# Optimization experiments

Measured on AMD Instinct MI355X. Metric: run time of the kernel, lower is better.

The kernel has to match this reference:

```python
import jax, jax.numpy as jnp
import numpy as np

D_MODEL = 1024
D_STATE = 16
LN_EPS = 1e-5


def setup_inputs() -> dict:
    key = jax.random.key(0)
    ks = jax.random.split(key, 8)
    batch, seq_len = 8, 4096
    x = jax.random.normal(ks[0], (batch, seq_len, D_MODEL), dtype=jnp.float32)
    A = jax.random.normal(ks[1], (D_STATE, D_STATE), dtype=jnp.float32) * 0.01
    # nn.Linear default init: U(-1/sqrt(fan_in), 1/sqrt(fan_in))
    bb = 1.0 / np.sqrt(D_MODEL)
    B_w = jax.random.uniform(ks[2], (D_STATE, D_MODEL), minval=-bb, maxval=bb)
    B_b = jax.random.uniform(ks[3], (D_STATE,), minval=-bb, maxval=bb)
    cb = 1.0 / np.sqrt(D_STATE)
    C_w = jax.random.uniform(ks[4], (D_MODEL, D_STATE), minval=-cb, maxval=cb)
    C_b = jax.random.uniform(ks[5], (D_MODEL,), minval=-cb, maxval=cb)
    D = jnp.ones((D_MODEL,), dtype=jnp.float32) * 0.01
    gate_w = jax.random.uniform(ks[6], (D_MODEL, D_MODEL), minval=-bb, maxval=bb)
    gate_b = jax.random.uniform(ks[7], (D_MODEL,), minval=-bb, maxval=bb)
    ln_g = jnp.ones((D_MODEL,), dtype=jnp.float32)
    ln_b = jnp.zeros((D_MODEL,), dtype=jnp.float32)
    return {"x": x, "A": A, "B_w": B_w, "B_b": B_b, "C_w": C_w, "C_b": C_b,
            "D": D, "gate_w": gate_w, "gate_b": gate_b, "ln_g": ln_g, "ln_b": ln_b}


def _layer_norm(z, g, b):
    mu = jnp.mean(z, axis=-1, keepdims=True)
    var = jnp.mean(jnp.square(z - mu), axis=-1, keepdims=True)
    return (z - mu) * jax.lax.rsqrt(var + LN_EPS) * g + b


def reference(x, A, B_w, B_b, C_w, C_b, D, gate_w, gate_b, ln_g, ln_b):
    batch, seq_len, d_model = x.shape
    # Precompute B(x_t) for all t in one GEMM: [b, s, d_state]
    Bx = jnp.einsum('bsd,nd->bsn', x, B_w) + B_b

    def step(state, bx_t):  # state: [b, d_state], bx_t: [b, d_state]
        new_state = jnp.tanh(state @ A.T + bx_t)
        return new_state, new_state

    init = jnp.zeros((batch, A.shape[0]), dtype=x.dtype)
    _, states = jax.lax.scan(step, init, jnp.swapaxes(Bx, 0, 1))  # [s, b, n]
    states = jnp.swapaxes(states, 0, 1)  # [b, s, d_state]

    output = jnp.einsum('bsn,dn->bsd', states, C_w) + C_b + D * x
    gate = jax.nn.silu(jnp.einsum('bsd,ed->bse', x, gate_w) + gate_b)
    output = gate * output + (1.0 - gate) * x
    return _layer_norm(output + x, ln_g, ln_b)
```

## Files before the change

kernel.cpp:

```cpp
#include <hip/hip_runtime.h>
#include <hip/hip_bf16.h>
#include <cstdint>
#include <cstddef>

#define DM     1024
#define DSTATE 16
#define SEQ    4096
#define BATCH  8
#define MROWS  (BATCH * SEQ)
#define LNEPS  1e-5f

#define CHUNK  64
#define WARM   16
#define NCHUNK (SEQ / CHUNK)

typedef __hip_bfloat16 bf16;
typedef __attribute__((ext_vector_type(8))) short short8;
typedef __attribute__((ext_vector_type(4))) float f32x4;

static __device__ __forceinline__ unsigned short f2bf(float f) {
  bf16 h = __float2bfloat16(f);
  return __builtin_bit_cast(unsigned short, h);
}

#define GLDS16(SRC, DSTOFF, LDSBASE)                                          \
  __builtin_amdgcn_global_load_lds(                                           \
      (const __attribute__((address_space(1))) void*)(SRC),                   \
      (__attribute__((address_space(3))) void*)((LDSBASE) + (DSTOFF)), 16, 0, 0)

#define WAITV(N) asm volatile("s_waitcnt vmcnt(" #N ")" ::: "memory")

#define XBLK (MROWS * DM / (256 * 8))
#define GBLK (DM * DM / (256 * 8))

__global__ __launch_bounds__(256) void canon_all(const float* __restrict__ xin,
                                                 const float* __restrict__ gw,
                                                 bf16* __restrict__ wsx,
                                                 bf16* __restrict__ gwc) {
  int blk = blockIdx.x;
  const float* src;
  bf16* dst;
  size_t i;
  if (blk < XBLK) {
    i = ((size_t)blk * 256 + threadIdx.x) * 8;
    src = xin; dst = wsx;
  } else {
    i = ((size_t)(blk - XBLK) * 256 + threadIdx.x) * 8;
    src = gw; dst = gwc;
  }
  const float4* p = (const float4*)(src + i);
  float4 a = p[0], b = p[1];
  uint4 o;
  o.x = (unsigned)f2bf(a.x) | ((unsigned)f2bf(a.y) << 16);
  o.y = (unsigned)f2bf(a.z) | ((unsigned)f2bf(a.w) << 16);
  o.z = (unsigned)f2bf(b.x) | ((unsigned)f2bf(b.y) << 16);
  o.w = (unsigned)f2bf(b.z) | ((unsigned)f2bf(b.w) << 16);
  *(uint4*)(dst + i) = o;
}

__global__ __launch_bounds__(256) void bx_kernel(const bf16* __restrict__ X,
                                                 const float* __restrict__ Bw,
                                                 const float* __restrict__ Bb,
                                                 float* __restrict__ Bx) {
  __shared__ __align__(16) char lds[40960];
  const int tid  = threadIdx.x;
  const int lane = tid & 63;
  const int w    = tid >> 6;
  const int fm   = lane & 15;
  const int fq   = lane >> 4;
  const int l4   = lane >> 2, lk = lane & 3;
  const int m0   = blockIdx.x * 64;

  {
    int t6   = tid & 63;
    int nb   = tid >> 6;
    int step = t6 >> 1;
    int cq0  = (t6 & 1) * 2;
#pragma unroll
    for (int p = 0; p < 4; ++p) {
      int n = p * 4 + nb;
      const float4* src = (const float4*)(Bw + (size_t)n * DM + t6 * 16);
      float4 a = src[0], b = src[1], c = src[2], d = src[3];
      uint4 o0, o1;
      o0.x = (unsigned)f2bf(a.x) | ((unsigned)f2bf(a.y) << 16);
      o0.y = (unsigned)f2bf(a.z) | ((unsigned)f2bf(a.w) << 16);
      o0.z = (unsigned)f2bf(b.x) | ((unsigned)f2bf(b.y) << 16);
      o0.w = (unsigned)f2bf(b.z) | ((unsigned)f2bf(b.w) << 16);
      o1.x = (unsigned)f2bf(c.x) | ((unsigned)f2bf(c.y) << 16);
      o1.y = (unsigned)f2bf(c.z) | ((unsigned)f2bf(c.w) << 16);
      o1.z = (unsigned)f2bf(d.x) | ((unsigned)f2bf(d.y) << 16);
      o1.w = (unsigned)f2bf(d.z) | ((unsigned)f2bf(d.w) << 16);
      int sw = (n >> 1) & 3;
      *(uint4*)(lds + step * 1024 + n * 64 + ((cq0 ^ sw) << 4))       = o0;
      *(uint4*)(lds + step * 1024 + n * 64 + (((cq0 + 1) ^ sw) << 4)) = o1;
    }
  }

  const int rowA = w * 16 + l4;
  const int kqA  = lk ^ ((rowA >> 1) & 3);
  GLDS16(X + (size_t)(m0 + rowA) * DM + kqA * 8, 32768 + w * 1024, lds);
  __syncthreads();

  const int rA   = w * 16 + fm;
  const int offA = rA * 64 + ((fq ^ ((rA >> 1) & 3)) << 4);
  const int offB = fm * 64 + ((fq ^ ((fm >> 1) & 3)) << 4);

  f32x4 acc = (f32x4)(0.f);
  for (int t = 0; t < 32; ++t) {
    const int cb = 32768 + (t & 1) * 4096;
    const int sb = 32768 + 4096 - (t & 1) * 4096;
    if (t < 31) {
      GLDS16(X + (size_t)(m0 + rowA) * DM + (t + 1) * 32 + kqA * 8,
             sb + w * 1024, lds);
      WAITV(1);
    } else {
      WAITV(0);
    }
    __builtin_amdgcn_s_barrier();
    __builtin_amdgcn_sched_barrier(0);
    short8 af  = *(const short8*)(lds + cb + offA);
    short8 bfv = *(const short8*)(lds + t * 1024 + offB);
    acc = __builtin_amdgcn_mfma_f32_16x16x32_bf16(af, bfv, acc, 0, 0, 0);
    __builtin_amdgcn_s_barrier();
  }
  float bb = Bb[fm];
#pragma unroll
  for (int q = 0; q < 4; ++q) {
    int row = m0 + w * 16 + fq * 4 + q;
    Bx[(size_t)row * DSTATE + fm] = acc[q] + bb;
  }
}

__global__ __launch_bounds__(64) void scan_kernel(const float* __restrict__ A,
                                                  const float* __restrict__ Bx,
                                                  float* __restrict__ st) {
  int lane = threadIdx.x;
  int n    = lane & 15;
  int base = lane & 48;
  int chain = blockIdx.x * 4 + (lane >> 4);
  int c = chain >> 3;
  int b = chain & 7;

  float Arow[16];
#pragma unroll
  for (int m = 0; m < 16; m++) Arow[m] = A[n * 16 + m];

  int t0   = (c == 0) ? 0 : c * CHUNK - WARM;
  int t1   = c * CHUNK;
  int tEnd = c * CHUNK + CHUNK;

  const float* bxp = Bx + (size_t)b * SEQ * DSTATE + n;
  float*       stp = st + (size_t)b * SEQ * DSTATE + n;

  float state = 0.f;
  for (int t = t0; t < tEnd; t++) {
    float a = bxp[(size_t)t * DSTATE];
#pragma unroll
    for (int m = 0; m < 16; m++)
      a += Arow[m] * __shfl(state, base + m, 64);
    float e = __expf(-2.f * fabsf(a));
    float r = (1.f - e) / (1.f + e);
    state = __builtin_copysignf(r, a);
    if (t >= t1) stp[(size_t)t * DSTATE] = state;
  }
}

#define FBM 32
#define FBK 32
#define NT  (DM / FBK)
#define BUFB 67584
#define CW_OFF 0
#define ST_OFF 65536
#define PART_OFF 67584
#define TOT_OFF 69632
#define BOUNCE 71680

__global__ __launch_bounds__(512, 2) void fused_kernel(
    const bf16* __restrict__ X, const bf16* __restrict__ Gw,
    const float* __restrict__ xf, const float* __restrict__ st,
    const float* __restrict__ Cw, const float* __restrict__ Cb,
    const float* __restrict__ Dv, const float* __restrict__ gb,
    const float* __restrict__ lng, const float* __restrict__ lnb,
    float* __restrict__ out) {
  __shared__ __align__(16) char lds[137216];
  const int tid  = threadIdx.x;
  const int lane = tid & 63;
  const int w    = tid >> 6;
  const int fm   = lane & 15;
  const int fq   = lane >> 4;
  const int m0   = blockIdx.x * FBM;
  const int l4   = lane >> 2, lk = lane & 3;

  int colS[8], kqS[8];
#pragma unroll
  for (int s = 0; s < 8; s++) {
    int col = (w * 8 + s) * 16 + l4;
    colS[s] = col;
    kqS[s]  = lk ^ ((col >> 1) & 3);
  }
  const int rowA = w * 16 + l4;
  const int kqA  = lk ^ ((rowA >> 1) & 3);

  int offA[2], offB[8];
#pragma unroll
  for (int i = 0; i < 2; i++) {
    int r = i * 16 + fm;
    offA[i] = r * 64 + ((fq ^ ((r >> 1) & 3)) << 4);
  }
#pragma unroll
  for (int j = 0; j < 8; j++) {
    int c = w * 128 + j * 16 + fm;
    offB[j] = 2048 + c * 64 + ((fq ^ ((c >> 1) & 3)) << 4);
  }

  f32x4 acc[2][8];
#pragma unroll
  for (int i = 0; i < 2; i++)
#pragma unroll
    for (int j = 0; j < 8; j++) acc[i][j] = (f32x4)(0.f);

  {
#pragma unroll
    for (int s = 0; s < 8; s++)
      GLDS16(Gw + (size_t)colS[s] * DM + kqS[s] * 8,
             2048 + (w * 8 + s) * 1024, lds);
    if (w < 2)
      GLDS16(X + (size_t)(m0 + rowA) * DM + kqA * 8, w * 1024, lds);
  }

  for (int t = 0; t < NT; t++) {
    const int cb = (t & 1) * BUFB;
    const int sb = BUFB - cb;
    if (t < NT - 1) {
      const int kb = (t + 1) * FBK;
#pragma unroll
      for (int s = 0; s < 8; s++)
        GLDS16(Gw + (size_t)colS[s] * DM + kb + kqS[s] * 8,
               sb + 2048 + (w * 8 + s) * 1024, lds);
      if (w < 2)
        GLDS16(X + (size_t)(m0 + rowA) * DM + kb + kqA * 8, sb + w * 1024, lds);
    } else {
#pragma unroll
      for (int s = 0; s < 8; s++) {
        int c   = w * 8 + s;
        int col = c * 16 + l4;
        int nq  = lk ^ ((col >> 1) & 3);
        GLDS16(Cw + (size_t)col * DSTATE + nq * 4, CW_OFF + c * 1024, lds);
      }
      if (w < 2) {
        int cc  = w;
        int row = cc * 16 + l4;
        int nq  = lk ^ ((row >> 1) & 3);
        GLDS16(st + (size_t)(m0 + row) * DSTATE + nq * 4, ST_OFF + cc * 1024, lds);
      }
    }

    if (w < 2) WAITV(9); else WAITV(8);
    __builtin_amdgcn_s_barrier();
    __builtin_amdgcn_sched_barrier(0);

    short8 af[2];
#pragma unroll
    for (int i = 0; i < 2; i++) af[i] = *(const short8*)(lds + cb + offA[i]);
#pragma unroll
    for (int j = 0; j < 8; j++) {
      short8 bfj = *(const short8*)(lds + cb + offB[j]);
#pragma unroll
      for (int i = 0; i < 2; i++)
        acc[i][j] = __builtin_amdgcn_mfma_f32_16x16x32_bf16(af[i], bfj,
                                                            acc[i][j], 0, 0, 0);
    }
    __builtin_amdgcn_s_barrier();
  }
  __syncthreads();

#pragma unroll
  for (int i = 0; i < 2; i++) {
    f32x4 stv[4][4];
#pragma unroll
    for (int nq = 0; nq < 4; nq++)
#pragma unroll
      for (int r = 0; r < 4; r++) {
        int row = i * 16 + fq * 4 + r;
        stv[nq][r] = *(const f32x4*)(lds + ST_OFF + row * 64 +
                                     ((nq ^ ((row >> 1) & 3)) << 4));
      }
    float sum4[4] = {0.f, 0.f, 0.f, 0.f};
    float ssq4[4] = {0.f, 0.f, 0.f, 0.f};
#pragma unroll
    for (int j = 0; j < 8; j++) {
      int c = w * 128 + j * 16 + fm;
      float oc[4] = {0.f, 0.f, 0.f, 0.f};
#pragma unroll
      for (int nq = 0; nq < 4; nq++) {
        f32x4 cw = *(const f32x4*)(lds + CW_OFF + c * 64 +
                                   ((nq ^ ((c >> 1) & 3)) << 4));
#pragma unroll
        for (int r = 0; r < 4; r++)
          oc[r] += stv[nq][r][0] * cw[0] + stv[nq][r][1] * cw[1] +
                   stv[nq][r][2] * cw[2] + stv[nq][r][3] * cw[3];
      }
      float gbv = gb[c], cbv = Cb[c], dvv = Dv[c];
#pragma unroll
      for (int r = 0; r < 4; r++) {
        int   grow = m0 + i * 16 + fq * 4 + r;
        float xv = xf[(size_t)grow * DM + c];
        float zg = acc[i][j][r] + gbv;
        float g  = zg / (1.f + __expf(-zg));
        float ocf = oc[r] + cbv + dvv * xv;
        float y  = g * ocf + (1.f - g) * xv;
        float z2 = y + xv;
        acc[i][j][r] = z2;
        sum4[r] += z2;
        ssq4[r] += z2 * z2;
      }
    }
#pragma unroll
    for (int r = 0; r < 4; r++) {
#pragma unroll
      for (int off = 1; off < 16; off <<= 1) {
        sum4[r] += __shfl_xor(sum4[r], off, 64);
        ssq4[r] += __shfl_xor(ssq4[r], off, 64);
      }
    }
    if (fm == 0) {
#pragma unroll
      for (int r = 0; r < 4; r++) {
        int row = i * 16 + fq * 4 + r;
        *(float2*)(lds + PART_OFF + w * 256 + row * 8) =
            make_float2(sum4[r], ssq4[r]);
      }
    }
  }
  __syncthreads();

  if (tid < 32) {
    float s = 0.f, q = 0.f;
#pragma unroll
    for (int ww = 0; ww < 8; ww++) {
      float2 p = *(const float2*)(lds + PART_OFF + ww * 256 + tid * 8);
      s += p.x; q += p.y;
    }
    float mu  = s * (1.f / DM);
    float var = q * (1.f / DM) - mu * mu;
    *(float2*)(lds + TOT_OFF + tid * 8) = make_float2(mu, rsqrtf(var + LNEPS));
  }
  __syncthreads();

  for (int h = 0; h < 2; ++h) {
#pragma unroll
    for (int j = 0; j < 8; ++j) {
      int c = w * 128 + j * 16 + fm;
#pragma unroll
      for (int r = 0; r < 4; ++r) {
        int row16 = fq * 4 + r;
        *(float*)(lds + BOUNCE + row16 * 4096 + c * 4) = acc[h][j][r];
      }
    }
    __syncthreads();
    {
      int row16 = tid >> 5;
      int lbase = (tid & 31) * 4;
      float2 mi = *(const float2*)(lds + TOT_OFF + (h * 16 + row16) * 8);
#pragma unroll
      for (int q = 0; q < 8; ++q) {
        int col = lbase + q * 128;
        f32x4 z = *(const f32x4*)(lds + BOUNCE + row16 * 4096 + col * 4);
        float4 g4 = *(const float4*)(lng + col);
        float4 b4 = *(const float4*)(lnb + col);
        float4 ov;
        ov.x = (z[0] - mi.x) * mi.y * g4.x + b4.x;
        ov.y = (z[1] - mi.x) * mi.y * g4.y + b4.y;
        ov.z = (z[2] - mi.x) * mi.y * g4.z + b4.z;
        ov.w = (z[3] - mi.x) * mi.y * g4.w + b4.w;
        *(float4*)(out + (size_t)(m0 + h * 16 + row16) * DM + col) = ov;
      }
    }
    __syncthreads();
  }
}

extern "C" void kernel_launch(void* const* d_in, const int* in_sizes, int n_in,
                              void* d_out, int out_size, void* d_ws, size_t ws_size,
                              hipStream_t stream) {
  (void)in_sizes; (void)n_in;
  const float* x   = (const float*)d_in[0];
  const float* A   = (const float*)d_in[1];
  const float* Bw  = (const float*)d_in[2];
  const float* Bb  = (const float*)d_in[3];
  const float* Cw  = (const float*)d_in[4];
  const float* Cb  = (const float*)d_in[5];
  const float* Dv  = (const float*)d_in[6];
  const float* Gw  = (const float*)d_in[7];
  const float* gb  = (const float*)d_in[8];
  const float* lng = (const float*)d_in[9];
  const float* lnb = (const float*)d_in[10];
  float* out = (float*)d_out;

  const size_t NEED = (size_t)72 << 20;
  if (ws_size < NEED) {
    hipMemsetAsync(d_out, 0, (size_t)out_size * 4, stream);
    return;
  }

  char* ws = (char*)d_ws;
  bf16*  wsx = (bf16*)(ws);
  bf16*  gwc = (bf16*)(ws + ((size_t)64 << 20));
  float* Bx  = (float*)(ws + ((size_t)66 << 20));
  float* st  = (float*)(ws + ((size_t)68 << 20));

  canon_all<<<XBLK + GBLK, 256, 0, stream>>>(x, Gw, wsx, gwc);
  bx_kernel<<<MROWS / 64, 256, 0, stream>>>(wsx, Bw, Bb, Bx);
  scan_kernel<<<(BATCH * NCHUNK) / 4, 64, 0, stream>>>(A, Bx, st);
  fused_kernel<<<MROWS / FBM, 512, 0, stream>>>(
      wsx, gwc, x, st, Cw, Cb, Dv, gb, lng, lnb, out);
}
```

Measured before the change: 500.0 us.

## Double fused GEMM row tile with 1024-thread blocks, halve scan chunk

The fused gate GEMM/epilogue kernel now processes 64 rows per block with 16 waves arranged as 2 row groups by 8 column groups. Each gate-weight K-slice loaded into LDS is shared by twice as many rows, which halves total weight traffic. In exchange, occupancy drops to one 1024-thread block per CU and the LN epilogue gets more passes. The scan chunk shrinks to 32, doubling parallel chains at the cost of more warm-up overhead. The bx kernel's explicit vmcnt wait plus double barrier is replaced by a single __syncthreads, which looks like it may drop the wait for the async global-to-LDS load.

```diff
diff --git a/kernel.cpp b/kernel.cpp
--- a/kernel.cpp
+++ b/kernel.cpp
@@ -10,7 +10,7 @@
 #define MROWS  (BATCH * SEQ)
 #define LNEPS  1e-5f
 
-#define CHUNK  64
+#define CHUNK  32
 #define WARM   16
 #define NCHUNK (SEQ / CHUNK)
 
@@ -109,19 +109,13 @@
   for (int t = 0; t < 32; ++t) {
     const int cb = 32768 + (t & 1) * 4096;
     const int sb = 32768 + 4096 - (t & 1) * 4096;
-    if (t < 31) {
+    if (t < 31)
       GLDS16(X + (size_t)(m0 + rowA) * DM + (t + 1) * 32 + kqA * 8,
              sb + w * 1024, lds);
-      WAITV(1);
-    } else {
-      WAITV(0);
-    }
-    __builtin_amdgcn_s_barrier();
-    __builtin_amdgcn_sched_barrier(0);
     short8 af  = *(const short8*)(lds + cb + offA);
     short8 bfv = *(const short8*)(lds + t * 1024 + offB);
     acc = __builtin_amdgcn_mfma_f32_16x16x32_bf16(af, bfv, acc, 0, 0, 0);
-    __builtin_amdgcn_s_barrier();
+    __syncthreads();
   }
   float bb = Bb[fm];
 #pragma unroll
@@ -165,36 +159,38 @@
   }
 }
 
-#define FBM 32
+#define FBM 64
 #define FBK 32
 #define NT  (DM / FBK)
-#define BUFB 67584
+#define BUFB 69632
 #define CW_OFF 0
 #define ST_OFF 65536
-#define PART_OFF 67584
-#define TOT_OFF 69632
-#define BOUNCE 71680
-
-__global__ __launch_bounds__(512, 2) void fused_kernel(
+#define BOUNCE 69632
+#define PART_OFF 139264
+#define TOT_OFF 143360
+
+__global__ __launch_bounds__(1024, 1) void fused_kernel(
     const bf16* __restrict__ X, const bf16* __restrict__ Gw,
     const float* __restrict__ xf, const float* __restrict__ st,
     const float* __restrict__ Cw, const float* __restrict__ Cb,
     const float* __restrict__ Dv, const float* __restrict__ gb,
     const float* __restrict__ lng, const float* __restrict__ lnb,
     float* __restrict__ out) {
-  __shared__ __align__(16) char lds[137216];
+  __shared__ __align__(16) char lds[143872];
   const int tid  = threadIdx.x;
   const int lane = tid & 63;
   const int w    = tid >> 6;
+  const int wr   = w >> 3;
+  const int wc   = w & 7;
   const int fm   = lane & 15;
   const int fq   = lane >> 4;
   const int m0   = blockIdx.x * FBM;
   const int l4   = lane >> 2, lk = lane & 3;
 
-  int colS[8], kqS[8];
-#pragma unroll
-  for (int s = 0; s < 8; s++) {
-    int col = (w * 8 + s) * 16 + l4;
+  int colS[4], kqS[4];
+#pragma unroll
+  for (int s = 0; s < 4; s++) {
+    int col = (w * 4 + s) * 16 + l4;
     colS[s] = col;
     kqS[s]  = lk ^ ((col >> 1) & 3);
   }
@@ -204,13 +200,13 @@
   int offA[2], offB[8];
 #pragma unroll
   for (int i = 0; i < 2; i++) {
-    int r = i * 16 + fm;
+    int r = wr * 32 + i * 16 + fm;
     offA[i] = r * 64 + ((fq ^ ((r >> 1) & 3)) << 4);
   }
 #pragma unroll
   for (int j = 0; j < 8; j++) {
-    int c = w * 128 + j * 16 + fm;
-    offB[j] = 2048 + c * 64 + ((fq ^ ((c >> 1) & 3)) << 4);
+    int c = wc * 128 + j * 16 + fm;
+    offB[j] = 4096 + c * 64 + ((fq ^ ((c >> 1) & 3)) << 4);
   }
 
   f32x4 acc[2][8];
@@ -221,10 +217,10 @@
 
   {
 #pragma unroll
-    for (int s = 0; s < 8; s++)
+    for (int s = 0; s < 4; s++)
       GLDS16(Gw + (size_t)colS[s] * DM + kqS[s] * 8,
-             2048 + (w * 8 + s) * 1024, lds);
-    if (w < 2)
+             4096 + (w * 4 + s) * 1024, lds);
+    if (w < 4)
       GLDS16(X + (size_t)(m0 + rowA) * DM + kqA * 8, w * 1024, lds);
   }
 
@@ -234,28 +230,27 @@
     if (t < NT - 1) {
       const int kb = (t + 1) * FBK;
 #pragma unroll
-      for (int s = 0; s < 8; s++)
+      for (int s = 0; s < 4; s++)
         GLDS16(Gw + (size_t)colS[s] * DM + kb + kqS[s] * 8,
-               sb + 2048 + (w * 8 + s) * 1024, lds);
-      if (w < 2)
+               sb + 4096 + (w * 4 + s) * 1024, lds);
+      if (w < 4)
         GLDS16(X + (size_t)(m0 + rowA) * DM + kb + kqA * 8, sb + w * 1024, lds);
     } else {
 #pragma unroll
-      for (int s = 0; s < 8; s++) {
-        int c   = w * 8 + s;
+      for (int s = 0; s < 4; s++) {
+        int c   = w * 4 + s;
         int col = c * 16 + l4;
         int nq  = lk ^ ((col >> 1) & 3);
         GLDS16(Cw + (size_t)col * DSTATE + nq * 4, CW_OFF + c * 1024, lds);
       }
-      if (w < 2) {
-        int cc  = w;
-        int row = cc * 16 + l4;
+      if (w < 4) {
+        int row = w * 16 + l4;
         int nq  = lk ^ ((row >> 1) & 3);
-        GLDS16(st + (size_t)(m0 + row) * DSTATE + nq * 4, ST_OFF + cc * 1024, lds);
-      }
-    }
-
-    if (w < 2) WAITV(9); else WAITV(8);
+        GLDS16(st + (size_t)(m0 + row) * DSTATE + nq * 4, ST_OFF + w * 1024, lds);
+      }
+    }
+
+    if (w < 4) WAITV(5); else WAITV(4);
     __builtin_amdgcn_s_barrier();
     __builtin_amdgcn_sched_barrier(0);
 
@@ -281,7 +276,7 @@
     for (int nq = 0; nq < 4; nq++)
 #pragma unroll
       for (int r = 0; r < 4; r++) {
-        int row = i * 16 + fq * 4 + r;
+        int row = wr * 32 + i * 16 + fq * 4 + r;
         stv[nq][r] = *(const f32x4*)(lds + ST_OFF + row * 64 +
                                      ((nq ^ ((row >> 1) & 3)) << 4));
       }
@@ -289,7 +284,7 @@
     float ssq4[4] = {0.f, 0.f, 0.f, 0.f};
 #pragma unroll
     for (int j = 0; j < 8; j++) {
-      int c = w * 128 + j * 16 + fm;
+      int c = wc * 128 + j * 16 + fm;
       float oc[4] = {0.f, 0.f, 0.f, 0.f};
 #pragma unroll
       for (int nq = 0; nq < 4; nq++) {
@@ -303,7 +298,7 @@
       float gbv = gb[c], cbv = Cb[c], dvv = Dv[c];
 #pragma unroll
       for (int r = 0; r < 4; r++) {
-        int   grow = m0 + i * 16 + fq * 4 + r;
+        int   grow = m0 + wr * 32 + i * 16 + fq * 4 + r;
         float xv = xf[(size_t)grow * DM + c];
         float zg = acc[i][j][r] + gbv;
         float g  = zg / (1.f + __expf(-zg));
@@ -334,11 +329,13 @@
   }
   __syncthreads();
 
-  if (tid < 32) {
+  if (tid < 64) {
+    int rw = tid >> 5;
     float s = 0.f, q = 0.f;
 #pragma unroll
-    for (int ww = 0; ww < 8; ww++) {
-      float2 p = *(const float2*)(lds + PART_OFF + ww * 256 + tid * 8);
+    for (int cc = 0; cc < 8; cc++) {
+      float2 p = *(const float2*)(lds + PART_OFF + (rw * 8 + cc) * 256 +
+                                  (tid & 31) * 8);
       s += p.x; q += p.y;
     }
     float mu  = s * (1.f / DM);
@@ -347,24 +344,27 @@
   }
   __syncthreads();
 
-  for (int h = 0; h < 2; ++h) {
-#pragma unroll
-    for (int j = 0; j < 8; ++j) {
-      int c = w * 128 + j * 16 + fm;
-#pragma unroll
-      for (int r = 0; r < 4; ++r) {
-        int row16 = fq * 4 + r;
-        *(float*)(lds + BOUNCE + row16 * 4096 + c * 4) = acc[h][j][r];
+  for (int h = 0; h < 4; ++h) {
+    if (wr == (h >> 1)) {
+      int i = h & 1;
+#pragma unroll
+      for (int j = 0; j < 8; ++j) {
+        int c = wc * 128 + j * 16 + fm;
+#pragma unroll
+        for (int r = 0; r < 4; ++r) {
+          int row16 = fq * 4 + r;
+          *(float*)(lds + BOUNCE + row16 * 4096 + c * 4) = acc[i][j][r];
+        }
       }
     }
     __syncthreads();
     {
-      int row16 = tid >> 5;
-      int lbase = (tid & 31) * 4;
+      int row16 = tid >> 6;
+      int lbase = (tid & 63) * 4;
       float2 mi = *(const float2*)(lds + TOT_OFF + (h * 16 + row16) * 8);
 #pragma unroll
-      for (int q = 0; q < 8; ++q) {
-        int col = lbase + q * 128;
+      for (int q = 0; q < 4; ++q) {
+        int col = lbase + q * 256;
         f32x4 z = *(const f32x4*)(lds + BOUNCE + row16 * 4096 + col * 4);
         float4 g4 = *(const float4*)(lng + col);
         float4 b4 = *(const float4*)(lnb + col);
@@ -412,6 +412,6 @@
   canon_all<<<XBLK + GBLK, 256, 0, stream>>>(x, Gw, wsx, gwc);
   bx_kernel<<<MROWS / 64, 256, 0, stream>>>(wsx, Bw, Bb, Bx);
   scan_kernel<<<(BATCH * NCHUNK) / 4, 64, 0, stream>>>(A, Bx, st);
-  fused_kernel<<<MROWS / FBM, 512, 0, stream>>>(
+  fused_kernel<<<MROWS / FBM, 1024, 0, stream>>>(
       wsx, gwc, x, st, Cw, Cb, Dv, gb, lng, lnb, out);
 }
```

Result: slower. 757.3 us (+51.5%).
